# Optimization experiments

Measured on AMD Instinct MI355X. Metric: run time of the kernel, lower is better.

## Reference

```python
import jax, jax.numpy as jnp
import numpy as np

DIM_MODEL = 1024
NHEAD = 16
DIM_HEAD = DIM_MODEL // NHEAD


def setup_inputs() -> dict:
    key = jax.random.key(0)
    k1, k2, k3, k4 = jax.random.split(key, 4)
    x = jax.random.normal(k1, (4, 2048, DIM_MODEL), dtype=jnp.float32)
    # nn.Linear weights: PyTorch stores [out, in]; we keep [in, out] for x @ W.
    s = 1.0 / np.sqrt(DIM_MODEL)
    w_qkv = jax.random.uniform(k2, (DIM_MODEL, 3 * DIM_MODEL), jnp.float32, -s, s)
    w_out = jax.random.uniform(k3, (DIM_MODEL, DIM_MODEL), jnp.float32, -s, s)
    b_out = jax.random.uniform(k4, (DIM_MODEL,), jnp.float32, -s, s)
    return {"x": x, "w_qkv": w_qkv, "w_out": w_out, "b_out": b_out}


def reference(x, w_qkv, w_out, b_out):
    b, n, _ = x.shape
    scale = DIM_HEAD ** -0.5
    qkv = x @ w_qkv                              # [b, n, 3*dim]
    q, k, v = jnp.split(qkv, 3, axis=-1)
    def split_heads(t):                          # [b, n, h*d] -> [b, h, n, d]
        return t.reshape(b, n, NHEAD, DIM_HEAD).transpose(0, 2, 1, 3)
    q, k, v = split_heads(q), split_heads(k), split_heads(v)
    attn = jnp.einsum('bhnd,bhmd->bhnm', q, k) * scale
    attn = jax.nn.softmax(attn, axis=-1)
    out = jnp.einsum('bhnm,bhmd->bhnd', attn, v)
    out = out.transpose(0, 2, 1, 3).reshape(b, n, NHEAD * DIM_HEAD)
    return out @ w_out + b_out
```

## Files before the change

### kernel.cpp

```cpp
#include <hip/hip_runtime.h>
#include <math.h>

#define DM   1024
#define NH   16
#define DH   64
#define SEQ  2048
#define BATCH 4
#define QSCALE 0.18033688011112042f

typedef __attribute__((ext_vector_type(8)))  short short8;
typedef __attribute__((ext_vector_type(4)))  float f32x4;
typedef __attribute__((ext_vector_type(16))) float f32x16;

static __device__ __forceinline__ unsigned short f2bf(float f) {
    unsigned u = __float_as_uint(f);
    unsigned r = (u + 0x7fffu + ((u >> 16) & 1u)) >> 16;
    return (unsigned short)r;
}

#define GLD(gp, lp) __builtin_amdgcn_global_load_lds( \
    (const __attribute__((address_space(1))) void*)(gp), \
    (__attribute__((address_space(3))) void*)(lp), 16, 0, 0)

__global__ __launch_bounds__(256) void cast_bf(
    const float* __restrict__ in, unsigned short* __restrict__ hi, int n4)
{
    int i = blockIdx.x * 256 + threadIdx.x;
    if (i >= n4) return;
    float4 v = reinterpret_cast<const float4*>(in)[i];
    ushort4 h;
    h.x = f2bf(v.x); h.y = f2bf(v.y); h.z = f2bf(v.z); h.w = f2bf(v.w);
    reinterpret_cast<ushort4*>(hi)[i] = h;
}

__global__ __launch_bounds__(256) void castT(
    const float* __restrict__ in, unsigned short* __restrict__ hiT, int K, int N)
{
    __shared__ float t[32][33];
    const int n0 = blockIdx.x * 32, k0 = blockIdx.y * 32;
    const int tx = threadIdx.x & 31, ty = threadIdx.x >> 5;
    #pragma unroll
    for (int r = 0; r < 32; r += 8)
        t[ty + r][tx] = in[(size_t)(k0 + ty + r) * N + n0 + tx];
    __syncthreads();
    #pragma unroll
    for (int r = 0; r < 32; r += 8)
        hiT[(size_t)(n0 + ty + r) * K + k0 + tx] = f2bf(t[tx][ty + r]);
}

__global__ __launch_bounds__(256) void gemm_qkv(
    const unsigned short* __restrict__ Ah, const unsigned short* __restrict__ Bh,
    unsigned short* __restrict__ Qh, unsigned short* __restrict__ Kph,
    unsigned short* __restrict__ Vph, int M, int N, int K)
{
    __shared__ __align__(16) unsigned short sAh[128 * 32];
    __shared__ __align__(16) unsigned short sBh[128 * 32];

    const int tid = threadIdx.x;
    const int l = tid & 63, w = tid >> 6;
    const int wr = w >> 1, wc = w & 1;

    int nwg = gridDim.x * gridDim.y;
    int lin = blockIdx.x + gridDim.x * blockIdx.y;
    int cpx = nwg >> 3;
    int nl = (lin & 7) * cpx + (lin >> 3);
    const int bm = (nl % gridDim.x) * 128, bn = (nl / gridDim.x) * 128;

    const int srow = w * 32 + (l >> 2);
    const int scol = (l & 3) * 8;
    const size_t a0 = (size_t)(bm + srow) * K + scol;
    const size_t a1 = (size_t)(bm + srow + 16) * K + scol;
    const size_t b0 = (size_t)(bn + srow) * K + scol;
    const size_t b1 = (size_t)(bn + srow + 16) * K + scol;

    const int fr = l & 15;
    const int fk = (l >> 4) * 8;

    f32x4 acc[4][4];
    #pragma unroll
    for (int i = 0; i < 4; ++i)
        #pragma unroll
        for (int j = 0; j < 4; ++j)
            acc[i][j] = (f32x4){0.f, 0.f, 0.f, 0.f};

    for (int k0 = 0; k0 < K; k0 += 32) {
        __syncthreads();
        GLD(Ah + a0 + k0, sAh + w * 1024);
        GLD(Ah + a1 + k0, sAh + w * 1024 + 512);
        GLD(Bh + b0 + k0, sBh + w * 1024);
        GLD(Bh + b1 + k0, sBh + w * 1024 + 512);
        __syncthreads();

        short8 vah[4], vbh[4];
        #pragma unroll
        for (int i = 0; i < 4; ++i) {
            int ar = (wr * 64 + i * 16 + fr) * 32 + fk;
            int br = (wc * 64 + i * 16 + fr) * 32 + fk;
            vah[i] = *reinterpret_cast<const short8*>(&sAh[ar]);
            vbh[i] = *reinterpret_cast<const short8*>(&sBh[br]);
        }
        __builtin_amdgcn_s_setprio(1);
        #pragma unroll
        for (int i = 0; i < 4; ++i)
            #pragma unroll
            for (int j = 0; j < 4; ++j)
                acc[i][j] = __builtin_amdgcn_mfma_f32_16x16x32_bf16(vah[i], vbh[j], acc[i][j], 0, 0, 0);
        __builtin_amdgcn_s_setprio(0);
    }

    #pragma unroll
    for (int i = 0; i < 4; ++i) {
        #pragma unroll
        for (int j = 0; j < 4; ++j) {
            int row0 = bm + wr * 64 + i * 16 + (l >> 4) * 4;
            int col  = bn + wc * 64 + j * 16 + fr;
            if (col < 1024) {
                #pragma unroll
                for (int r = 0; r < 4; ++r)
                    Qh[(size_t)(row0 + r) * 1024 + col] = f2bf(acc[i][j][r] * QSCALE);
            } else if (col < 2048) {
                int sec = col - 1024, head = sec >> 6, d = sec & 63;
                int pK = ((d >> 4) << 1) | ((d >> 3) & 1);
                int d7 = d & 7;
                #pragma unroll
                for (int r = 0; r < 4; ++r) {
                    int row = row0 + r;
                    int bb = row >> 11, seq = row & 2047;
                    int kt = seq >> 6, k64 = seq & 63;
                    int p = ((k64 >> 5) << 3) + pK;
                    size_t addr = ((((size_t)(bb * 16 + head) * 32 + kt) * 512)
                                   + p * 32 + (k64 & 31)) * 8 + d7;
                    Kph[addr] = f2bf(acc[i][j][r]);
                }
            } else {
                int sec = col - 2048, head = sec >> 6, d = sec & 63;
                int row = row0;
                int bb = row >> 11, seq = row & 2047;
                int kt = seq >> 6, k64 = seq & 63, k16 = k64 & 15;
                int p = ((d >> 5) << 3) + ((k64 >> 4) << 1) + ((k16 >> 2) & 1);
                int jbase = (k16 >> 3) << 2;
                size_t chunk = (((size_t)(bb * 16 + head) * 32 + kt) * 512
                                + p * 32 + (d & 31));
                ushort4 v4;
                #pragma unroll
                for (int r = 0; r < 4; ++r)
                    ((unsigned short*)&v4)[r] = f2bf(acc[i][j][r]);
                *reinterpret_cast<ushort4*>(Vph + chunk * 8 + jbase) = v4;
            }
        }
    }
}

__global__ __launch_bounds__(256) void gemm_out(
    const unsigned short* __restrict__ Ah, const unsigned short* __restrict__ Bh,
    const float* __restrict__ bias, float* __restrict__ C, int M, int N, int K)
{
    __shared__ __align__(16) unsigned short sAh[128 * 32];
    __shared__ __align__(16) unsigned short sBh[128 * 32];

    const int tid = threadIdx.x;
    const int l = tid & 63, w = tid >> 6;
    const int wr = w >> 1, wc = w & 1;

    int nwg = gridDim.x * gridDim.y;
    int lin = blockIdx.x + gridDim.x * blockIdx.y;
    int cpx = nwg >> 3;
    int nl = (lin & 7) * cpx + (lin >> 3);
    const int bm = (nl % gridDim.x) * 128, bn = (nl / gridDim.x) * 128;

    const int srow = w * 32 + (l >> 2);
    const int scol = (l & 3) * 8;
    const size_t a0 = (size_t)(bm + srow) * K + scol;
    const size_t a1 = (size_t)(bm + srow + 16) * K + scol;
    const size_t b0 = (size_t)(bn + srow) * K + scol;
    const size_t b1 = (size_t)(bn + srow + 16) * K + scol;

    const int fr = l & 15;
    const int fk = (l >> 4) * 8;

    f32x4 acc[4][4];
    #pragma unroll
    for (int i = 0; i < 4; ++i)
        #pragma unroll
        for (int j = 0; j < 4; ++j)
            acc[i][j] = (f32x4){0.f, 0.f, 0.f, 0.f};

    for (int k0 = 0; k0 < K; k0 += 32) {
        __syncthreads();
        GLD(Ah + a0 + k0, sAh + w * 1024);
        GLD(Ah + a1 + k0, sAh + w * 1024 + 512);
        GLD(Bh + b0 + k0, sBh + w * 1024);
        GLD(Bh + b1 + k0, sBh + w * 1024 + 512);
        __syncthreads();

        short8 vah[4], vbh[4];
        #pragma unroll
        for (int i = 0; i < 4; ++i) {
            int ar = (wr * 64 + i * 16 + fr) * 32 + fk;
            int br = (wc * 64 + i * 16 + fr) * 32 + fk;
            vah[i] = *reinterpret_cast<const short8*>(&sAh[ar]);
            vbh[i] = *reinterpret_cast<const short8*>(&sBh[br]);
        }
        __builtin_amdgcn_s_setprio(1);
        #pragma unroll
        for (int i = 0; i < 4; ++i)
            #pragma unroll
            for (int j = 0; j < 4; ++j)
                acc[i][j] = __builtin_amdgcn_mfma_f32_16x16x32_bf16(vah[i], vbh[j], acc[i][j], 0, 0, 0);
        __builtin_amdgcn_s_setprio(0);
    }

    #pragma unroll
    for (int i = 0; i < 4; ++i) {
        #pragma unroll
        for (int j = 0; j < 4; ++j) {
            int row = bm + wr * 64 + i * 16 + (l >> 4) * 4;
            int col = bn + wc * 64 + j * 16 + fr;
            float bb = bias[col];
            #pragma unroll
            for (int r = 0; r < 4; ++r)
                C[(size_t)(row + r) * N + col] = acc[i][j][r] + bb;
        }
    }
}

__global__ __launch_bounds__(256, 3) void flash_attn_mfma(
    const unsigned short* __restrict__ Qh,
    const unsigned short* __restrict__ Kph,
    const unsigned short* __restrict__ Vph,
    unsigned short* __restrict__ out_hi)
{
    __shared__ __align__(16) unsigned short sK[2][4096];
    __shared__ __align__(16) unsigned short sV[3][4096];

    int lin = blockIdx.x + 16 * blockIdx.y + 256 * blockIdx.z;
    int nlid = (lin & 7) * 128 + (lin >> 3);
    const int qt = nlid & 15, head = (nlid >> 4) & 15, b = nlid >> 8;

    const int tid = threadIdx.x;
    const int l = tid & 63, w = tid >> 6;
    const int q5 = l & 31, hf = l >> 5;

    const int bh = b * NH + head;
    const size_t kvb = (size_t)bh * 32 * 512 * 8;

    #define STAGE_K(cbuf, kt_) do {                                           \
        _Pragma("unroll")                                                     \
        for (int i2 = 0; i2 < 2; ++i2) {                                      \
            int ch = (w * 2 + i2) * 64 + l;                                   \
            GLD(Kph + kvb + ((size_t)(kt_) * 512 + ch) * 8,                   \
                (char*)&sK[cbuf][0] + ch * 16);                               \
        }                                                                     \
    } while (0)

    #define STAGE_V(vbuf, kt_) do {                                           \
        _Pragma("unroll")                                                     \
        for (int i2 = 0; i2 < 2; ++i2) {                                      \
            int ch = (w * 2 + i2) * 64 + l;                                   \
            GLD(Vph + kvb + ((size_t)(kt_) * 512 + ch) * 8,                   \
                (char*)&sV[vbuf][0] + ch * 16);                               \
        }                                                                     \
    } while (0)

    const int qrow = qt * 128 + w * 32 + q5;
    short8 qhr[4];
    {
        const size_t qb = ((size_t)b * SEQ + qrow) * 1024 + head * 64;
        #pragma unroll
        for (int s = 0; s < 4; ++s)
            qhr[s] = *reinterpret_cast<const short8*>(Qh + qb + s * 16 + hf * 8);
    }

    float l_ = 0.f;
    f32x16 oacc0, oacc1, sacc0, sacc1;
    #pragma unroll
    for (int r = 0; r < 16; ++r) { oacc0[r] = 0.f; oacc1[r] = 0.f; }

    union FragU { unsigned u[4]; short8 s8; };
    short8 pbh[4];

    #define QK(kt_) do {                                                      \
        const char* kb = (const char*)&sK[(kt_) & 1][0] + l * 16;             \
        _Pragma("unroll")                                                     \
        for (int r = 0; r < 16; ++r) { sacc0[r] = 0.f; sacc1[r] = 0.f; }      \
        __builtin_amdgcn_s_setprio(1);                                        \
        _Pragma("unroll")                                                     \
        for (int s = 0; s < 4; ++s) {                                         \
            short8 k0h = *reinterpret_cast<const short8*>(kb + s * 1024);     \
            short8 k1h = *reinterpret_cast<const short8*>(kb + (4 + s) * 1024); \
            sacc0 = __builtin_amdgcn_mfma_f32_32x32x16_bf16(k0h, qhr[s], sacc0, 0, 0, 0); \
            sacc1 = __builtin_amdgcn_mfma_f32_32x32x16_bf16(k1h, qhr[s], sacc1, 0, 0, 0); \
        }                                                                     \
        __builtin_amdgcn_s_setprio(0);                                        \
    } while (0)

    #define PV(vbuf_) do {                                                    \
        const char* vb = (const char*)&sV[vbuf_][0] + l * 16;                 \
        __builtin_amdgcn_s_setprio(1);                                        \
        _Pragma("unroll")                                                     \
        for (int kpv = 0; kpv < 4; ++kpv) {                                   \
            short8 v0h = *reinterpret_cast<const short8*>(vb + kpv * 1024);   \
            short8 v1h = *reinterpret_cast<const short8*>(vb + (4 + kpv) * 1024); \
            oacc0 = __builtin_amdgcn_mfma_f32_32x32x16_bf16(v0h, pbh[kpv], oacc0, 0, 0, 0); \
            oacc1 = __builtin_amdgcn_mfma_f32_32x32x16_bf16(v1h, pbh[kpv], oacc1, 0, 0, 0); \
        }                                                                     \
        __builtin_amdgcn_s_setprio(0);                                        \
    } while (0)

    #define EXPPACK() do {                                                    \
        float ssum = 0.f;                                                     \
        _Pragma("unroll")                                                     \
        for (int jt = 0; jt < 2; ++jt) {                                      \
            float pv[16];                                                     \
            _Pragma("unroll")                                                 \
            for (int r = 0; r < 16; ++r) {                                    \
                float sv = (jt == 0) ? sacc0[r] : sacc1[r];                   \
                pv[r] = __builtin_amdgcn_exp2f(sv);                           \
                ssum += pv[r];                                                \
            }                                                                 \
            FragU f0, f1;                                                     \
            asm("v_cvt_pk_bf16_f32 %0, %1, %2" : "=v"(f0.u[0]) : "v"(pv[0]),  "v"(pv[1])); \
            asm("v_cvt_pk_bf16_f32 %0, %1, %2" : "=v"(f0.u[1]) : "v"(pv[2]),  "v"(pv[3])); \
            asm("v_cvt_pk_bf16_f32 %0, %1, %2" : "=v"(f0.u[2]) : "v"(pv[4]),  "v"(pv[5])); \
            asm("v_cvt_pk_bf16_f32 %0, %1, %2" : "=v"(f0.u[3]) : "v"(pv[6]),  "v"(pv[7])); \
            asm("v_cvt_pk_bf16_f32 %0, %1, %2" : "=v"(f1.u[0]) : "v"(pv[8]),  "v"(pv[9])); \
            asm("v_cvt_pk_bf16_f32 %0, %1, %2" : "=v"(f1.u[1]) : "v"(pv[10]), "v"(pv[11])); \
            asm("v_cvt_pk_bf16_f32 %0, %1, %2" : "=v"(f1.u[2]) : "v"(pv[12]), "v"(pv[13])); \
            asm("v_cvt_pk_bf16_f32 %0, %1, %2" : "=v"(f1.u[3]) : "v"(pv[14]), "v"(pv[15])); \
            pbh[jt * 2 + 0] = f0.s8;                                          \
            pbh[jt * 2 + 1] = f1.s8;                                          \
        }                                                                     \
        ssum += __shfl_xor(ssum, 32);                                         \
        l_ += ssum;                                                           \
    } while (0)

    STAGE_K(0, 0); STAGE_V(0, 0);
    __syncthreads();
    STAGE_K(1, 1); STAGE_V(1, 1);
    QK(0);
    EXPPACK();

    for (int kt = 1; kt < SEQ / 64; ++kt) {
        __syncthreads();
        if (kt + 1 < SEQ / 64) {
            STAGE_K((kt + 1) & 1, kt + 1);
            STAGE_V((kt + 1) % 3, kt + 1);
        }
        QK(kt);
        PV((kt - 1) % 3);
        EXPPACK();
    }
    PV((SEQ / 64 - 1) % 3);

    float linv = 1.f / l_;
    #pragma unroll
    for (int dt = 0; dt < 2; ++dt) {
        #pragma unroll
        for (int rq = 0; rq < 4; ++rq) {
            int dbase = dt * 32 + rq * 8 + 4 * hf;
            ushort4 h4;
            #pragma unroll
            for (int c = 0; c < 4; ++c) {
                float v = ((dt == 0) ? oacc0[rq * 4 + c] : oacc1[rq * 4 + c]) * linv;
                ((unsigned short*)&h4)[c] = f2bf(v);
            }
            size_t o = ((size_t)b * SEQ + qrow) * DM + head * 64 + dbase;
            *reinterpret_cast<ushort4*>(out_hi + o) = h4;
        }
    }
    #undef STAGE_K
    #undef STAGE_V
    #undef QK
    #undef PV
    #undef EXPPACK
}

extern "C" void kernel_launch(void* const* d_in, const int* in_sizes, int n_in,
                              void* d_out, int out_size, void* d_ws, size_t ws_size,
                              hipStream_t stream) {
    const float* x     = (const float*)d_in[0];
    const float* w_qkv = (const float*)d_in[1];
    const float* w_out = (const float*)d_in[2];
    const float* b_out = (const float*)d_in[3];
    float* out = (float*)d_out;

    const int M = BATCH * SEQ;

    char* ws = (char*)d_ws;
    unsigned short* x_h   = (unsigned short*)ws;                         ws += (size_t)M * DM * 2;
    unsigned short* Qh    = (unsigned short*)ws;                         ws += (size_t)M * DM * 2;
    unsigned short* Kp_h  = (unsigned short*)ws;                         ws += (size_t)M * DM * 2;
    unsigned short* Vp_h  = (unsigned short*)ws;                         ws += (size_t)M * DM * 2;
    unsigned short* wqT_h = (unsigned short*)ws;                         ws += (size_t)3072 * DM * 2;
    unsigned short* woT_h = (unsigned short*)ws;                         ws += (size_t)DM * DM * 2;
    unsigned short* at_hi = (unsigned short*)ws;

    dim3 blk(256);

    cast_bf<<<dim3(M * DM / 4 / 256), blk, 0, stream>>>(x, x_h, M * DM / 4);
    castT<<<dim3(3072 / 32, DM / 32), blk, 0, stream>>>(w_qkv, wqT_h, DM, 3 * DM);
    castT<<<dim3(DM / 32, DM / 32), blk, 0, stream>>>(w_out, woT_h, DM, DM);

    gemm_qkv<<<dim3(M / 128, 3 * DM / 128), blk, 0, stream>>>(
        x_h, wqT_h, Qh, Kp_h, Vp_h, M, 3 * DM, DM);

    flash_attn_mfma<<<dim3(SEQ / 128, NH, BATCH), blk, 0, stream>>>(
        Qh, Kp_h, Vp_h, at_hi);

    gemm_out<<<dim3(M / 128, DM / 128), blk, 0, stream>>>(
        at_hi, woT_h, b_out, out, M, DM, DM);
}
```

Baseline: 204.4 us.

## Fuse cast kernels, vectorize GEMM epilogues, simplify attention KV pipeline

Merges the three input/weight cast and transpose kernels into a single launch to cut launch overhead. For the Q, K and output GEMMs it swaps the MFMA operand order so each lane holds four consecutive columns, which lets the epilogues issue 8-byte and 16-byte vector stores instead of scalar ones. The flash attention kernel drops its software-pipelined QK/PV overlap and triple-buffered V, and instead stages K and V together into double buffers and runs QK, exp and PV back to back each iteration. That reduces LDS use and code complexity but loses the overlap between QK and PV.

```diff
diff --git a/kernel.cpp b/kernel.cpp
--- a/kernel.cpp
+++ b/kernel.cpp
@@ -22,30 +22,42 @@
     (const __attribute__((address_space(1))) void*)(gp), \
     (__attribute__((address_space(3))) void*)(lp), 16, 0, 0)
 
-__global__ __launch_bounds__(256) void cast_bf(
-    const float* __restrict__ in, unsigned short* __restrict__ hi, int n4)
-{
-    int i = blockIdx.x * 256 + threadIdx.x;
-    if (i >= n4) return;
-    float4 v = reinterpret_cast<const float4*>(in)[i];
-    ushort4 h;
-    h.x = f2bf(v.x); h.y = f2bf(v.y); h.z = f2bf(v.z); h.w = f2bf(v.w);
-    reinterpret_cast<ushort4*>(hi)[i] = h;
-}
-
-__global__ __launch_bounds__(256) void castT(
-    const float* __restrict__ in, unsigned short* __restrict__ hiT, int K, int N)
+__global__ __launch_bounds__(256) void prep_all(
+    const float* __restrict__ x, unsigned short* __restrict__ x_h,
+    const float* __restrict__ w_qkv, unsigned short* __restrict__ wqT_h,
+    const float* __restrict__ w_out, unsigned short* __restrict__ woT_h)
 {
     __shared__ float t[32][33];
-    const int n0 = blockIdx.x * 32, k0 = blockIdx.y * 32;
-    const int tx = threadIdx.x & 31, ty = threadIdx.x >> 5;
+    const int bid = blockIdx.x;
+    const int tid = threadIdx.x;
+    if (bid < 8192) {
+        int i = bid * 256 + tid;
+        float4 v = reinterpret_cast<const float4*>(x)[i];
+        ushort4 h;
+        h.x = f2bf(v.x); h.y = f2bf(v.y); h.z = f2bf(v.z); h.w = f2bf(v.w);
+        reinterpret_cast<ushort4*>(x_h)[i] = h;
+        return;
+    }
+    const float* in;
+    unsigned short* outT;
+    int K = DM, N, n0, k0;
+    if (bid < 8192 + 3072) {
+        int bb = bid - 8192;
+        in = w_qkv; outT = wqT_h; N = 3 * DM;
+        n0 = (bb % 96) * 32; k0 = (bb / 96) * 32;
+    } else {
+        int bb = bid - 8192 - 3072;
+        in = w_out; outT = woT_h; N = DM;
+        n0 = (bb % 32) * 32; k0 = (bb / 32) * 32;
+    }
+    const int tx = tid & 31, ty = tid >> 5;
     #pragma unroll
     for (int r = 0; r < 32; r += 8)
         t[ty + r][tx] = in[(size_t)(k0 + ty + r) * N + n0 + tx];
     __syncthreads();
     #pragma unroll
     for (int r = 0; r < 32; r += 8)
-        hiT[(size_t)(n0 + ty + r) * K + k0 + tx] = f2bf(t[tx][ty + r]);
+        outT[(size_t)(n0 + ty + r) * K + k0 + tx] = f2bf(t[tx][ty + r]);
 }
 
 __global__ __launch_bounds__(256) void gemm_qkv(
@@ -65,6 +77,7 @@
     int cpx = nwg >> 3;
     int nl = (lin & 7) * cpx + (lin >> 3);
     const int bm = (nl % gridDim.x) * 128, bn = (nl / gridDim.x) * 128;
+    const bool swap = (bn < 2048);
 
     const int srow = w * 32 + (l >> 2);
     const int scol = (l & 3) * 8;
@@ -100,42 +113,65 @@
             vbh[i] = *reinterpret_cast<const short8*>(&sBh[br]);
         }
         __builtin_amdgcn_s_setprio(1);
-        #pragma unroll
-        for (int i = 0; i < 4; ++i)
-            #pragma unroll
-            for (int j = 0; j < 4; ++j)
-                acc[i][j] = __builtin_amdgcn_mfma_f32_16x16x32_bf16(vah[i], vbh[j], acc[i][j], 0, 0, 0);
+        if (swap) {
+            #pragma unroll
+            for (int i = 0; i < 4; ++i)
+                #pragma unroll
+                for (int j = 0; j < 4; ++j)
+                    acc[i][j] = __builtin_amdgcn_mfma_f32_16x16x32_bf16(vbh[j], vah[i], acc[i][j], 0, 0, 0);
+        } else {
+            #pragma unroll
+            for (int i = 0; i < 4; ++i)
+                #pragma unroll
+                for (int j = 0; j < 4; ++j)
+                    acc[i][j] = __builtin_amdgcn_mfma_f32_16x16x32_bf16(vah[i], vbh[j], acc[i][j], 0, 0, 0);
+        }
         __builtin_amdgcn_s_setprio(0);
     }
 
-    #pragma unroll
-    for (int i = 0; i < 4; ++i) {
-        #pragma unroll
-        for (int j = 0; j < 4; ++j) {
-            int row0 = bm + wr * 64 + i * 16 + (l >> 4) * 4;
-            int col  = bn + wc * 64 + j * 16 + fr;
-            if (col < 1024) {
+    if (bn < 1024) {
+        #pragma unroll
+        for (int i = 0; i < 4; ++i) {
+            int seq = bm + wr * 64 + i * 16 + fr;
+            #pragma unroll
+            for (int j = 0; j < 4; ++j) {
+                int col = bn + wc * 64 + j * 16 + (l >> 4) * 4;
+                ushort4 q4;
                 #pragma unroll
                 for (int r = 0; r < 4; ++r)
-                    Qh[(size_t)(row0 + r) * 1024 + col] = f2bf(acc[i][j][r] * QSCALE);
-            } else if (col < 2048) {
-                int sec = col - 1024, head = sec >> 6, d = sec & 63;
-                int pK = ((d >> 4) << 1) | ((d >> 3) & 1);
-                int d7 = d & 7;
+                    ((unsigned short*)&q4)[r] = f2bf(acc[i][j][r] * QSCALE);
+                *reinterpret_cast<ushort4*>(Qh + (size_t)seq * 1024 + col) = q4;
+            }
+        }
+    } else if (bn < 2048) {
+        #pragma unroll
+        for (int i = 0; i < 4; ++i) {
+            int seq_g = bm + wr * 64 + i * 16 + fr;
+            int bb = seq_g >> 11, s2 = seq_g & 2047;
+            int kt = s2 >> 6, k64 = s2 & 63;
+            #pragma unroll
+            for (int j = 0; j < 4; ++j) {
+                int d_base = (bn - 1024) + wc * 64 + j * 16 + (l >> 4) * 4;
+                int head = d_base >> 6, d = d_base & 63;
+                int p = ((k64 >> 5) << 3) + ((d >> 4) << 1) + ((d >> 3) & 1);
+                size_t addr = ((((size_t)(bb * 16 + head) * 32 + kt) * 512)
+                               + p * 32 + (k64 & 31)) * 8 + (d & 7);
+                ushort4 k4;
                 #pragma unroll
-                for (int r = 0; r < 4; ++r) {
-                    int row = row0 + r;
-                    int bb = row >> 11, seq = row & 2047;
-                    int kt = seq >> 6, k64 = seq & 63;
-                    int p = ((k64 >> 5) << 3) + pK;
-                    size_t addr = ((((size_t)(bb * 16 + head) * 32 + kt) * 512)
-                                   + p * 32 + (k64 & 31)) * 8 + d7;
-                    Kph[addr] = f2bf(acc[i][j][r]);
-                }
-            } else {
+                for (int r = 0; r < 4; ++r)
+                    ((unsigned short*)&k4)[r] = f2bf(acc[i][j][r]);
+                *reinterpret_cast<ushort4*>(Kph + addr) = k4;
+            }
+        }
+    } else {
+        #pragma unroll
+        for (int i = 0; i < 4; ++i) {
+            #pragma unroll
+            for (int j = 0; j < 4; ++j) {
+                int row0 = bm + wr * 64 + i * 16 + (l >> 4) * 4;
+                int col  = bn + wc * 64 + j * 16 + fr;
                 int sec = col - 2048, head = sec >> 6, d = sec & 63;
-                int row = row0;
-                int bb = row >> 11, seq = row & 2047;
+                int bb = row0 >> 11, seq = row0 & 2047;
                 int kt = seq >> 6, k64 = seq & 63, k16 = k64 & 15;
                 int p = ((d >> 5) << 3) + ((k64 >> 4) << 1) + ((k16 >> 2) & 1);
                 int jbase = (k16 >> 3) << 2;
@@ -206,20 +242,21 @@
         for (int i = 0; i < 4; ++i)
             #pragma unroll
             for (int j = 0; j < 4; ++j)
-                acc[i][j] = __builtin_amdgcn_mfma_f32_16x16x32_bf16(vah[i], vbh[j], acc[i][j], 0, 0, 0);
+                acc[i][j] = __builtin_amdgcn_mfma_f32_16x16x32_bf16(vbh[j], vah[i], acc[i][j], 0, 0, 0);
         __builtin_amdgcn_s_setprio(0);
     }
 
     #pragma unroll
     for (int i = 0; i < 4; ++i) {
+        int seq = bm + wr * 64 + i * 16 + fr;
         #pragma unroll
         for (int j = 0; j < 4; ++j) {
-            int row = bm + wr * 64 + i * 16 + (l >> 4) * 4;
-            int col = bn + wc * 64 + j * 16 + fr;
-            float bb = bias[col];
-            #pragma unroll
-            for (int r = 0; r < 4; ++r)
-                C[(size_t)(row + r) * N + col] = acc[i][j][r] + bb;
+            int col = bn + wc * 64 + j * 16 + (l >> 4) * 4;
+            float4 bb = *reinterpret_cast<const float4*>(bias + col);
+            float4 o;
+            o.x = acc[i][j][0] + bb.x; o.y = acc[i][j][1] + bb.y;
+            o.z = acc[i][j][2] + bb.z; o.w = acc[i][j][3] + bb.w;
+            *reinterpret_cast<float4*>(C + (size_t)seq * N + col) = o;
         }
     }
 }
@@ -231,7 +268,7 @@
     unsigned short* __restrict__ out_hi)
 {
     __shared__ __align__(16) unsigned short sK[2][4096];
-    __shared__ __align__(16) unsigned short sV[3][4096];
+    __shared__ __align__(16) unsigned short sV[2][4096];
 
     int lin = blockIdx.x + 16 * blockIdx.y + 256 * blockIdx.z;
     int nlid = (lin & 7) * 128 + (lin >> 3);
@@ -244,21 +281,13 @@
     const int bh = b * NH + head;
     const size_t kvb = (size_t)bh * 32 * 512 * 8;
 
-    #define STAGE_K(cbuf, kt_) do {                                           \
+    #define STAGE_KV(cbuf, kt_) do {                                          \
         _Pragma("unroll")                                                     \
         for (int i2 = 0; i2 < 2; ++i2) {                                      \
             int ch = (w * 2 + i2) * 64 + l;                                   \
-            GLD(Kph + kvb + ((size_t)(kt_) * 512 + ch) * 8,                   \
-                (char*)&sK[cbuf][0] + ch * 16);                               \
-        }                                                                     \
-    } while (0)
-
-    #define STAGE_V(vbuf, kt_) do {                                           \
-        _Pragma("unroll")                                                     \
-        for (int i2 = 0; i2 < 2; ++i2) {                                      \
-            int ch = (w * 2 + i2) * 64 + l;                                   \
-            GLD(Vph + kvb + ((size_t)(kt_) * 512 + ch) * 8,                   \
-                (char*)&sV[vbuf][0] + ch * 16);                               \
+            size_t s8 = kvb + ((size_t)(kt_) * 512 + ch) * 8;                 \
+            GLD(Kph + s8, (char*)&sK[cbuf][0] + ch * 16);                     \
+            GLD(Vph + s8, (char*)&sV[cbuf][0] + ch * 16);                     \
         }                                                                     \
     } while (0)
 
@@ -272,86 +301,73 @@
     }
 
     float l_ = 0.f;
-    f32x16 oacc0, oacc1, sacc0, sacc1;
+    f32x16 oacc0, oacc1;
     #pragma unroll
     for (int r = 0; r < 16; ++r) { oacc0[r] = 0.f; oacc1[r] = 0.f; }
 
     union FragU { unsigned u[4]; short8 s8; };
     short8 pbh[4];
 
-    #define QK(kt_) do {                                                      \
-        const char* kb = (const char*)&sK[(kt_) & 1][0] + l * 16;             \
-        _Pragma("unroll")                                                     \
-        for (int r = 0; r < 16; ++r) { sacc0[r] = 0.f; sacc1[r] = 0.f; }      \
-        __builtin_amdgcn_s_setprio(1);                                        \
-        _Pragma("unroll")                                                     \
-        for (int s = 0; s < 4; ++s) {                                         \
-            short8 k0h = *reinterpret_cast<const short8*>(kb + s * 1024);     \
-            short8 k1h = *reinterpret_cast<const short8*>(kb + (4 + s) * 1024); \
-            sacc0 = __builtin_amdgcn_mfma_f32_32x32x16_bf16(k0h, qhr[s], sacc0, 0, 0, 0); \
-            sacc1 = __builtin_amdgcn_mfma_f32_32x32x16_bf16(k1h, qhr[s], sacc1, 0, 0, 0); \
-        }                                                                     \
-        __builtin_amdgcn_s_setprio(0);                                        \
-    } while (0)
-
-    #define PV(vbuf_) do {                                                    \
-        const char* vb = (const char*)&sV[vbuf_][0] + l * 16;                 \
-        __builtin_amdgcn_s_setprio(1);                                        \
-        _Pragma("unroll")                                                     \
-        for (int kpv = 0; kpv < 4; ++kpv) {                                   \
-            short8 v0h = *reinterpret_cast<const short8*>(vb + kpv * 1024);   \
-            short8 v1h = *reinterpret_cast<const short8*>(vb + (4 + kpv) * 1024); \
-            oacc0 = __builtin_amdgcn_mfma_f32_32x32x16_bf16(v0h, pbh[kpv], oacc0, 0, 0, 0); \
-            oacc1 = __builtin_amdgcn_mfma_f32_32x32x16_bf16(v1h, pbh[kpv], oacc1, 0, 0, 0); \
-        }                                                                     \
-        __builtin_amdgcn_s_setprio(0);                                        \
-    } while (0)
-
-    #define EXPPACK() do {                                                    \
-        float ssum = 0.f;                                                     \
-        _Pragma("unroll")                                                     \
-        for (int jt = 0; jt < 2; ++jt) {                                      \
-            float pv[16];                                                     \
-            _Pragma("unroll")                                                 \
-            for (int r = 0; r < 16; ++r) {                                    \
-                float sv = (jt == 0) ? sacc0[r] : sacc1[r];                   \
-                pv[r] = __builtin_amdgcn_exp2f(sv);                           \
-                ssum += pv[r];                                                \
-            }                                                                 \
-            FragU f0, f1;                                                     \
-            asm("v_cvt_pk_bf16_f32 %0, %1, %2" : "=v"(f0.u[0]) : "v"(pv[0]),  "v"(pv[1])); \
-            asm("v_cvt_pk_bf16_f32 %0, %1, %2" : "=v"(f0.u[1]) : "v"(pv[2]),  "v"(pv[3])); \
-            asm("v_cvt_pk_bf16_f32 %0, %1, %2" : "=v"(f0.u[2]) : "v"(pv[4]),  "v"(pv[5])); \
-            asm("v_cvt_pk_bf16_f32 %0, %1, %2" : "=v"(f0.u[3]) : "v"(pv[6]),  "v"(pv[7])); \
-            asm("v_cvt_pk_bf16_f32 %0, %1, %2" : "=v"(f1.u[0]) : "v"(pv[8]),  "v"(pv[9])); \
-            asm("v_cvt_pk_bf16_f32 %0, %1, %2" : "=v"(f1.u[1]) : "v"(pv[10]), "v"(pv[11])); \
-            asm("v_cvt_pk_bf16_f32 %0, %1, %2" : "=v"(f1.u[2]) : "v"(pv[12]), "v"(pv[13])); \
-            asm("v_cvt_pk_bf16_f32 %0, %1, %2" : "=v"(f1.u[3]) : "v"(pv[14]), "v"(pv[15])); \
-            pbh[jt * 2 + 0] = f0.s8;                                          \
-            pbh[jt * 2 + 1] = f1.s8;                                          \
-        }                                                                     \
-        ssum += __shfl_xor(ssum, 32);                                         \
-        l_ += ssum;                                                           \
-    } while (0)
-
-    STAGE_K(0, 0); STAGE_V(0, 0);
-    __syncthreads();
-    STAGE_K(1, 1); STAGE_V(1, 1);
-    QK(0);
-    EXPPACK();
-
-    for (int kt = 1; kt < SEQ / 64; ++kt) {
+    STAGE_KV(0, 0);
+    int cur = 0;
+
+    for (int kt = 0; kt < SEQ / 64; ++kt) {
         __syncthreads();
-        if (kt + 1 < SEQ / 64) {
-            STAGE_K((kt + 1) & 1, kt + 1);
-            STAGE_V((kt + 1) % 3, kt + 1);
-        }
-        QK(kt);
-        PV((kt - 1) % 3);
-        EXPPACK();
-    }
-    PV((SEQ / 64 - 1) % 3);
-
+        if (kt + 1 < SEQ / 64) STAGE_KV(cur ^ 1, kt + 1);
+
+        const char* kb = (const char*)&sK[cur][0] + l * 16;
+
+        f32x16 sacc0, sacc1;
+        #pragma unroll
+        for (int r = 0; r < 16; ++r) { sacc0[r] = 0.f; sacc1[r] = 0.f; }
+        __builtin_amdgcn_s_setprio(1);
+        #pragma unroll
+        for (int s = 0; s < 4; ++s) {
+            short8 k0h = *reinterpret_cast<const short8*>(kb + s * 1024);
+            short8 k1h = *reinterpret_cast<const short8*>(kb + (4 + s) * 1024);
+            sacc0 = __builtin_amdgcn_mfma_f32_32x32x16_bf16(k0h, qhr[s], sacc0, 0, 0, 0);
+            sacc1 = __builtin_amdgcn_mfma_f32_32x32x16_bf16(k1h, qhr[s], sacc1, 0, 0, 0);
+        }
+        __builtin_amdgcn_s_setprio(0);
+
+        float ssum = 0.f;
+        #pragma unroll
+        for (int jt = 0; jt < 2; ++jt) {
+            float pv[16];
+            #pragma unroll
+            for (int r = 0; r < 16; ++r) {
+                float sv = (jt == 0) ? sacc0[r] : sacc1[r];
+                pv[r] = __builtin_amdgcn_exp2f(sv);
+                ssum += pv[r];
+            }
+            FragU f0, f1;
+            asm("v_cvt_pk_bf16_f32 %0, %1, %2" : "=v"(f0.u[0]) : "v"(pv[0]),  "v"(pv[1]));
+            asm("v_cvt_pk_bf16_f32 %0, %1, %2" : "=v"(f0.u[1]) : "v"(pv[2]),  "v"(pv[3]));
+            asm("v_cvt_pk_bf16_f32 %0, %1, %2" : "=v"(f0.u[2]) : "v"(pv[4]),  "v"(pv[5]));
+            asm("v_cvt_pk_bf16_f32 %0, %1, %2" : "=v"(f0.u[3]) : "v"(pv[6]),  "v"(pv[7]));
+            asm("v_cvt_pk_bf16_f32 %0, %1, %2" : "=v"(f1.u[0]) : "v"(pv[8]),  "v"(pv[9]));
+            asm("v_cvt_pk_bf16_f32 %0, %1, %2" : "=v"(f1.u[1]) : "v"(pv[10]), "v"(pv[11]));
+            asm("v_cvt_pk_bf16_f32 %0, %1, %2" : "=v"(f1.u[2]) : "v"(pv[12]), "v"(pv[13]));
+            asm("v_cvt_pk_bf16_f32 %0, %1, %2" : "=v"(f1.u[3]) : "v"(pv[14]), "v"(pv[15]));
+            pbh[jt * 2 + 0] = f0.s8;
+            pbh[jt * 2 + 1] = f1.s8;
+        }
+        l_ += ssum;
+
+        const char* vb = (const char*)&sV[cur][0] + l * 16;
+        __builtin_amdgcn_s_setprio(1);
+        #pragma unroll
+        for (int kpv = 0; kpv < 4; ++kpv) {
+            short8 v0h = *reinterpret_cast<const short8*>(vb + kpv * 1024);
+            short8 v1h = *reinterpret_cast<const short8*>(vb + (4 + kpv) * 1024);
+            oacc0 = __builtin_amdgcn_mfma_f32_32x32x16_bf16(v0h, pbh[kpv], oacc0, 0, 0, 0);
+            oacc1 = __builtin_amdgcn_mfma_f32_32x32x16_bf16(v1h, pbh[kpv], oacc1, 0, 0, 0);
+        }
+        __builtin_amdgcn_s_setprio(0);
+        cur ^= 1;
+    }
+
+    l_ += __shfl_xor(l_, 32);
     float linv = 1.f / l_;
     #pragma unroll
     for (int dt = 0; dt < 2; ++dt) {
@@ -368,11 +384,7 @@
             *reinterpret_cast<ushort4*>(out_hi + o) = h4;
         }
     }
-    #undef STAGE_K
-    #undef STAGE_V
-    #undef QK
-    #undef PV
-    #undef EXPPACK
+    #undef STAGE_KV
 }
 
 extern "C" void kernel_launch(void* const* d_in, const int* in_sizes, int n_in,
@@ -397,9 +409,8 @@
 
     dim3 blk(256);
 
-    cast_bf<<<dim3(M * DM / 4 / 256), blk, 0, stream>>>(x, x_h, M * DM / 4);
-    castT<<<dim3(3072 / 32, DM / 32), blk, 0, stream>>>(w_qkv, wqT_h, DM, 3 * DM);
-    castT<<<dim3(DM / 32, DM / 32), blk, 0, stream>>>(w_out, woT_h, DM, DM);
+    prep_all<<<dim3(8192 + 3072 + 1024), blk, 0, stream>>>(
+        x, x_h, w_qkv, wqT_h, w_out, woT_h);
 
     gemm_qkv<<<dim3(M / 128, 3 * DM / 128), blk, 0, stream>>>(
         x_h, wqT_h, Qh, Kp_h, Vp_h, M, 3 * DM, DM);
```

Result: slower. 287.3 us (+40.5%).
